# Kernel tuning notes

Measured on AMD Instinct MI355X. Metric: run time of the kernel, lower is better.

Reference implementation:

```python
import jax, jax.numpy as jnp
import numpy as np

B, H, S, D = 4, 16, 2048, 128
HIDDEN_DIM = 128  # init arg; used as softmax scale


def setup_inputs() -> dict:
    key = jax.random.key(0)
    kq, kk, kv = jax.random.split(key, 3)
    q = jax.random.normal(kq, (B, H, S, D), dtype=jnp.float32)
    k = jax.random.normal(kk, (B, H, S, D), dtype=jnp.float32)
    v = jax.random.normal(kv, (B, H, S, D), dtype=jnp.float32)
    return {"q": q, "k": k, "v": v}


def reference(q, k, v):
    # scores[b,h,s,t] = sum_d q[b,h,s,d] * k[b,h,t,d]  (y permuted on last two dims, then matmul)
    scores = jnp.einsum("bhsd,bhtd->bhst", q, k) * (HIDDEN_DIM ** -0.5)
    probs = jax.nn.softmax(scores, axis=-1)
    return jnp.einsum("bhst,bhtd->bhsd", probs, v)
```

## Files before the change

### kernel.cpp

```cpp
#include <hip/hip_runtime.h>
#include <hip/hip_bf16.h>


#define SEQ 2048
#define DH  128
#define NBH 64
#define BM  128
#define BN  64
#define NT  (SEQ / BN)
#define QK_LD 136
#define VT_LD 72
#define P_LD  72
#define TP_LD 130
#define THR 8.0f

typedef __attribute__((ext_vector_type(8))) short short8;
typedef __attribute__((ext_vector_type(4))) float f32x4;
typedef __attribute__((ext_vector_type(16))) float f32x16;
typedef __attribute__((ext_vector_type(2))) unsigned int u32x2;

#if __has_builtin(__builtin_amdgcn_exp2f)
#define EXP2F(x) __builtin_amdgcn_exp2f(x)
#else
#define EXP2F(x) exp2f(x)
#endif

#define CS (0.08838834764831845f * 1.44269504088896340736f)

__device__ __forceinline__ unsigned int pk_bf16(float lo, float hi) {
    union { __hip_bfloat162 h; unsigned int u; } cv;
    cv.h = __float22bfloat162_rn(make_float2(lo, hi));
    return cv.u;
}

__device__ __forceinline__ short8 repack_pf(float a0, float a1, float a2, float a3,
                                            float a4, float a5, float a6, float a7,
                                            int hi) {
    unsigned pq0 = pk_bf16(a0, a1);
    unsigned pq1 = pk_bf16(a2, a3);
    unsigned pq2 = pk_bf16(a4, a5);
    unsigned pq3 = pk_bf16(a6, a7);
    union { short8 s; uint4 u; } cv;
#if __has_builtin(__builtin_amdgcn_permlane32_swap)
    u32x2 r02 = __builtin_amdgcn_permlane32_swap(pq0, pq2, false, false);
    u32x2 r13 = __builtin_amdgcn_permlane32_swap(pq1, pq3, false, false);
    cv.u.x = r02[0]; cv.u.y = r13[0]; cv.u.z = r02[1]; cv.u.w = r13[1];
    (void)hi;
#else
    unsigned px0 = (unsigned)__shfl_xor((int)pq0, 32);
    unsigned px1 = (unsigned)__shfl_xor((int)pq1, 32);
    unsigned px2 = (unsigned)__shfl_xor((int)pq2, 32);
    unsigned px3 = (unsigned)__shfl_xor((int)pq3, 32);
    cv.u.x = hi ? px2 : pq0;
    cv.u.y = hi ? px3 : pq1;
    cv.u.z = hi ? pq2 : px0;
    cv.u.w = hi ? pq3 : px1;
#endif
    return cv.s;
}

template<bool DOK>
__global__ __launch_bounds__(256) void prep_kernel(
        const float* __restrict__ v, unsigned short* __restrict__ vt,
        const float* __restrict__ k, unsigned short* __restrict__ kb) {
    __shared__ unsigned int tileT[64 * TP_LD];
    const int tid = threadIdx.x;

    if (blockIdx.x >= 8) {
        if (!DOK) return;
        const int kid = (blockIdx.x - 8) + 8 * blockIdx.y + 16 * blockIdx.z;
        const float* src = k + (size_t)kid * 16384;
        unsigned short* dst = kb + (size_t)kid * 16384;
#pragma unroll
        for (int i = 0; i < 16; ++i) {
            int off = (tid + 256 * i) * 4;
            float4 val = *reinterpret_cast<const float4*>(src + off);
            uint2 pk;
            pk.x = pk_bf16(val.x, val.y);
            pk.y = pk_bf16(val.z, val.w);
            *reinterpret_cast<uint2*>(dst + off) = pk;
        }
        return;
    }

    const int bh = blockIdx.z;
    const int s0 = blockIdx.x * 256;
    const int d0 = blockIdx.y * 64;
    const int lane = tid & 63;
    const int wv   = tid >> 6;
    const int l31  = lane & 31;
    const int hiv  = lane >> 5;

    const float* srcv = v + ((size_t)bh * SEQ + s0) * DH + d0 + 2 * l31;
    const int drow = 2 * l31 + hiv;
#pragma unroll 4
    for (int i = 0; i < 32; ++i) {
        const int kp = wv * 32 + i;
        float2 X = *reinterpret_cast<const float2*>(srcv + (size_t)(2 * kp + hiv) * DH);
        union { float f; unsigned u; } bx, by;
        bx.f = X.x; by.f = X.y;
        float k0d0, k1d0, k0d1, k1d1;
#if __has_builtin(__builtin_amdgcn_permlane32_swap)
        u32x2 rx = __builtin_amdgcn_permlane32_swap(bx.u, bx.u, false, false);
        u32x2 ry = __builtin_amdgcn_permlane32_swap(by.u, by.u, false, false);
        union { unsigned u; float f; } c0, c1, c2, c3;
        c0.u = rx[0]; c1.u = rx[1]; c2.u = ry[0]; c3.u = ry[1];
        k0d0 = c0.f; k1d0 = c1.f; k0d1 = c2.f; k1d1 = c3.f;
#else
        float xo = __shfl_xor(X.x, 32), yo = __shfl_xor(X.y, 32);
        k0d0 = hiv ? xo : X.x;  k1d0 = hiv ? X.x : xo;
        k0d1 = hiv ? yo : X.y;  k1d1 = hiv ? X.y : yo;
#endif
        unsigned pk = hiv ? pk_bf16(k0d1, k1d1) : pk_bf16(k0d0, k1d0);
        tileT[drow * TP_LD + kp] = pk;
    }
    __syncthreads();

    unsigned short* dst = vt + ((size_t)bh * DH + d0) * SEQ + s0;
#pragma unroll
    for (int i = 0; i < 8; ++i) {
        int id = tid + 256 * i;
        int dd = id >> 5;
        int m  = id & 31;
        const unsigned int* p = &tileT[dd * TP_LD + 4 * m];
        uint2 a = *reinterpret_cast<const uint2*>(p);
        uint2 b = *reinterpret_cast<const uint2*>(p + 2);
        uint4 o; o.x = a.x; o.y = a.y; o.z = b.x; o.w = b.y;
        *reinterpret_cast<uint4*>(dst + (size_t)dd * SEQ + 8 * m) = o;
    }
}

__global__ __launch_bounds__(256, 2) void fattn_kernel(
        const float* __restrict__ q, const unsigned short* __restrict__ kb,
        const unsigned short* __restrict__ vt, float* __restrict__ out) {
    __shared__ unsigned short Ks[2][BN * QK_LD];
    __shared__ unsigned short Vs[2][DH * VT_LD];

    const int wid = ((blockIdx.x & 7) << 7) | (blockIdx.x >> 3);
    const int bh  = wid >> 4;
    const int q0  = (wid & 15) * BM;
    const int tid  = threadIdx.x;
    const int w    = tid >> 6;
    const int lane = tid & 63;
    const int l31  = lane & 31;
    const int hi   = lane >> 5;

    short8 qb[8];
    {
        const float* qptr = q + ((size_t)bh * SEQ + q0 + w * 32 + l31) * DH + hi * 8;
#pragma unroll
        for (int ks = 0; ks < 8; ++ks) {
            float4 x = *reinterpret_cast<const float4*>(qptr + 16 * ks);
            float4 y = *reinterpret_cast<const float4*>(qptr + 16 * ks + 4);
            union { short8 s; uint4 u; } cv;
            cv.u.x = pk_bf16(x.x * CS, x.y * CS);
            cv.u.y = pk_bf16(x.z * CS, x.w * CS);
            cv.u.z = pk_bf16(y.x * CS, y.y * CS);
            cv.u.w = pk_bf16(y.z * CS, y.w * CS);
            qb[ks] = cv.s;
        }
    }

    f32x16 o0, o1, o2, o3;
#pragma unroll
    for (int i = 0; i < 16; ++i) { o0[i] = 0.f; o1[i] = 0.f; o2[i] = 0.f; o3[i] = 0.f; }
    float m = -1e30f, lsum = 0.f;

    const unsigned short* kbp  = kb + (size_t)bh * SEQ * DH;
    const unsigned short* vptr = vt + (size_t)bh * DH * SEQ;

    uint4 kr0, kr1, kr2, kr3, vr0, vr1, vr2, vr3;
    const int krow = tid >> 4, kcol = (tid & 15) << 3;
    const int vrow = tid >> 3, vcol = (tid & 7) << 3;
    const unsigned short* kst = kbp + (size_t)krow * DH + kcol;
    const unsigned short* vst = vptr + (size_t)vrow * SEQ + vcol;

#define LOAD_TILE(K0)                                                              \
    do {                                                                           \
        const unsigned short* _kp = kst + (size_t)(K0) * DH;                       \
        kr0 = *reinterpret_cast<const uint4*>(_kp);                                \
        kr1 = *reinterpret_cast<const uint4*>(_kp + 16 * DH);                      \
        kr2 = *reinterpret_cast<const uint4*>(_kp + 32 * DH);                      \
        kr3 = *reinterpret_cast<const uint4*>(_kp + 48 * DH);                      \
        const unsigned short* _vp = vst + (K0);                                    \
        vr0 = *reinterpret_cast<const uint4*>(_vp);                                \
        vr1 = *reinterpret_cast<const uint4*>(_vp + 32 * SEQ);                     \
        vr2 = *reinterpret_cast<const uint4*>(_vp + 64 * SEQ);                     \
        vr3 = *reinterpret_cast<const uint4*>(_vp + 96 * SEQ);                     \
    } while (0)

#define WRITE_TILE(B)                                                              \
    do {                                                                           \
        *reinterpret_cast<uint4*>(&Ks[B][(krow     ) * QK_LD + kcol]) = kr0;       \
        *reinterpret_cast<uint4*>(&Ks[B][(krow + 16) * QK_LD + kcol]) = kr1;       \
        *reinterpret_cast<uint4*>(&Ks[B][(krow + 32) * QK_LD + kcol]) = kr2;       \
        *reinterpret_cast<uint4*>(&Ks[B][(krow + 48) * QK_LD + kcol]) = kr3;       \
        *reinterpret_cast<uint4*>(&Vs[B][(vrow     ) * VT_LD + vcol]) = vr0;       \
        *reinterpret_cast<uint4*>(&Vs[B][(vrow + 32) * VT_LD + vcol]) = vr1;       \
        *reinterpret_cast<uint4*>(&Vs[B][(vrow + 64) * VT_LD + vcol]) = vr2;       \
        *reinterpret_cast<uint4*>(&Vs[B][(vrow + 96) * VT_LD + vcol]) = vr3;       \
    } while (0)

    LOAD_TILE(0);
    WRITE_TILE(0);
    __syncthreads();
    int cur = 0;

    for (int kt = 0; kt < NT; ++kt) {
        if (kt + 1 < NT) LOAD_TILE((kt + 1) * BN);

        const unsigned short* KsA = &Ks[cur][l31 * QK_LD + hi * 8];
        const unsigned short* VsA = &Vs[cur][l31 * VT_LD + hi * 8];

        f32x16 s0, s1;
#pragma unroll
        for (int i = 0; i < 16; ++i) { s0[i] = 0.f; s1[i] = 0.f; }
        __builtin_amdgcn_s_setprio(1);
#pragma unroll
        for (int ks = 0; ks < 8; ++ks) {
            short8 a0 = *reinterpret_cast<const short8*>(KsA + 16 * ks);
            short8 a1 = *reinterpret_cast<const short8*>(KsA + 32 * QK_LD + 16 * ks);
            s0 = __builtin_amdgcn_mfma_f32_32x32x16_bf16(a0, qb[ks], s0, 0, 0, 0);
            s1 = __builtin_amdgcn_mfma_f32_32x32x16_bf16(a1, qb[ks], s1, 0, 0, 0);
        }
        __builtin_amdgcn_s_setprio(0);

        float mx = s0[0];
#pragma unroll
        for (int i = 1; i < 16; ++i) mx = fmaxf(mx, s0[i]);
#pragma unroll
        for (int i = 0; i < 16; ++i) mx = fmaxf(mx, s1[i]);
        mx = fmaxf(mx, __shfl_xor(mx, 32));
        if (__any(mx - m > THR)) {
            float mn = fmaxf(m, mx);
            float al = EXP2F(m - mn);
            m = mn; lsum *= al;
#pragma unroll
            for (int i = 0; i < 16; ++i) { o0[i] *= al; o1[i] *= al; o2[i] *= al; o3[i] *= al; }
        }
#pragma unroll
        for (int i = 0; i < 16; ++i) s0[i] = EXP2F(s0[i] - m);
#pragma unroll
        for (int i = 0; i < 16; ++i) s1[i] = EXP2F(s1[i] - m);
        float ls = 0.f;
#pragma unroll
        for (int i = 0; i < 16; ++i) ls += s0[i] + s1[i];
        lsum += ls;

        short8 pf0 = repack_pf(s0[0], s0[1], s0[2],  s0[3],  s0[4],  s0[5],  s0[6],  s0[7],  hi);
        short8 pf1 = repack_pf(s0[8], s0[9], s0[10], s0[11], s0[12], s0[13], s0[14], s0[15], hi);
        short8 pf2 = repack_pf(s1[0], s1[1], s1[2],  s1[3],  s1[4],  s1[5],  s1[6],  s1[7],  hi);
        short8 pf3 = repack_pf(s1[8], s1[9], s1[10], s1[11], s1[12], s1[13], s1[14], s1[15], hi);

        __builtin_amdgcn_s_setprio(1);
#define PV_C(OC, C)                                                                \
        {                                                                          \
            short8 va0 = *reinterpret_cast<const short8*>(VsA + (32*(C)) * VT_LD);      \
            short8 va1 = *reinterpret_cast<const short8*>(VsA + (32*(C)) * VT_LD + 16); \
            short8 va2 = *reinterpret_cast<const short8*>(VsA + (32*(C)) * VT_LD + 32); \
            short8 va3 = *reinterpret_cast<const short8*>(VsA + (32*(C)) * VT_LD + 48); \
            OC = __builtin_amdgcn_mfma_f32_32x32x16_bf16(va0, pf0, OC, 0, 0, 0);   \
            OC = __builtin_amdgcn_mfma_f32_32x32x16_bf16(va1, pf1, OC, 0, 0, 0);   \
            OC = __builtin_amdgcn_mfma_f32_32x32x16_bf16(va2, pf2, OC, 0, 0, 0);   \
            OC = __builtin_amdgcn_mfma_f32_32x32x16_bf16(va3, pf3, OC, 0, 0, 0);   \
        }
        PV_C(o0, 0) PV_C(o1, 1) PV_C(o2, 2) PV_C(o3, 3)
        __builtin_amdgcn_s_setprio(0);

        if (kt + 1 < NT) WRITE_TILE(cur ^ 1);
        __syncthreads();
        cur ^= 1;
    }

    lsum += __shfl_xor(lsum, 32);
    float inv = 1.0f / lsum;
    float* obase = out + ((size_t)bh * SEQ + q0 + w * 32 + l31) * DH + 4 * hi;
#define STORE_C(OC, C)                                                             \
    {                                                                              \
        _Pragma("unroll")                                                          \
        for (int u = 0; u < 4; ++u) {                                              \
            float4 st;                                                             \
            st.x = OC[4*u+0] * inv; st.y = OC[4*u+1] * inv;                        \
            st.z = OC[4*u+2] * inv; st.w = OC[4*u+3] * inv;                        \
            *reinterpret_cast<float4*>(obase + 32*(C) + 8*u) = st;                 \
        }                                                                          \
    }
    STORE_C(o0, 0) STORE_C(o1, 1) STORE_C(o2, 2) STORE_C(o3, 3)
}

__global__ __launch_bounds__(256, 3) void fattn_fallback(
        const float* __restrict__ q, const float* __restrict__ kf,
        const unsigned short* __restrict__ vt, float* __restrict__ out) {
    __shared__ unsigned short Ks[64 * QK_LD];
    __shared__ unsigned short Vs[DH * VT_LD];
    __shared__ unsigned short Ps[64 * P_LD];

    const int wid = ((blockIdx.x & 7) << 8) | (blockIdx.x >> 3);
    const int bh  = wid >> 5;
    const int q0  = (wid & 31) * 64;
    const int tid  = threadIdx.x;
    const int w    = tid >> 6;
    const int lane = tid & 63;
    const int l15  = lane & 15;
    const int quad = lane >> 4;

    short8 qf[4];
    {
        const float* qptr = q + ((size_t)bh * SEQ + q0 + w * 16 + l15) * DH + quad * 8;
#pragma unroll
        for (int kk = 0; kk < 4; ++kk) {
            float4 x = *reinterpret_cast<const float4*>(qptr + kk * 32);
            float4 y = *reinterpret_cast<const float4*>(qptr + kk * 32 + 4);
            union { short8 s; uint4 u; } cv;
            cv.u.x = pk_bf16(x.x * CS, x.y * CS);
            cv.u.y = pk_bf16(x.z * CS, x.w * CS);
            cv.u.z = pk_bf16(y.x * CS, y.y * CS);
            cv.u.w = pk_bf16(y.z * CS, y.w * CS);
            qf[kk] = cv.s;
        }
    }

    f32x4 o[8];
#pragma unroll
    for (int t = 0; t < 8; ++t) o[t] = (f32x4){0.f, 0.f, 0.f, 0.f};
    float mrow[4] = {-1e30f, -1e30f, -1e30f, -1e30f};
    float lrow[4] = {0.f, 0.f, 0.f, 0.f};

    const float*          kfp  = kf + (size_t)bh * SEQ * DH;
    const unsigned short* vptr = vt + (size_t)bh * DH * SEQ;

    unsigned int* Ps32 = reinterpret_cast<unsigned int*>(Ps);
    const int prow_base = w * 16 + quad * 4;
    const int pdw = (l15 & 1) ? (8 + (l15 >> 1)) : (l15 >> 1);

    for (int kt = 0; kt < NT; ++kt) {
        const int k0 = kt * BN;
#pragma unroll
        for (int i = 0; i < 8; ++i) {
            int id  = tid + 256 * i;
            int row = id >> 5;
            int c4  = (id & 31) << 2;
            float4 val = *reinterpret_cast<const float4*>(kfp + (size_t)(k0 + row) * DH + c4);
            uint2 pk;
            pk.x = pk_bf16(val.x, val.y);
            pk.y = pk_bf16(val.z, val.w);
            *reinterpret_cast<uint2*>(&Ks[row * QK_LD + c4]) = pk;
        }
#pragma unroll
        for (int i = 0; i < 4; ++i) {
            int id = tid + 256 * i;
            int dd = id >> 3;
            int kc = (id & 7) << 3;
            *reinterpret_cast<uint4*>(&Vs[dd * VT_LD + kc]) =
                *reinterpret_cast<const uint4*>(vptr + (size_t)dd * SEQ + k0 + kc);
        }
        __syncthreads();

        f32x4 acc[4];
#pragma unroll
        for (int t = 0; t < 4; ++t) acc[t] = (f32x4){0.f, 0.f, 0.f, 0.f};
#pragma unroll
        for (int kk = 0; kk < 4; ++kk) {
            const int koff = kk * 32 + quad * 8;
#pragma unroll
            for (int t = 0; t < 4; ++t) {
                short8 b = *reinterpret_cast<const short8*>(&Ks[(t * 16 + l15) * QK_LD + koff]);
                acc[t] = __builtin_amdgcn_mfma_f32_16x16x32_bf16(qf[kk], b, acc[t], 0, 0, 0);
            }
        }

        float lm[4];
#pragma unroll
        for (int r = 0; r < 4; ++r)
            lm[r] = fmaxf(fmaxf(acc[0][r], acc[1][r]), fmaxf(acc[2][r], acc[3][r]));
        float need = fmaxf(fmaxf(lm[0] - mrow[0], lm[1] - mrow[1]),
                           fmaxf(lm[2] - mrow[2], lm[3] - mrow[3]));
        if (__any(need > THR)) {
#pragma unroll
            for (int r = 0; r < 4; ++r) {
                float mx = lm[r];
#pragma unroll
                for (int off = 1; off < 16; off <<= 1)
                    mx = fmaxf(mx, __shfl_xor(mx, off));
                float mnew  = fmaxf(mrow[r], mx);
                float alpha = EXP2F(mrow[r] - mnew);
                mrow[r] = mnew;
                lrow[r] *= alpha;
#pragma unroll
                for (int t = 0; t < 8; ++t) o[t][r] *= alpha;
            }
        }

#pragma unroll
        for (int r = 0; r < 4; ++r) {
            float p0 = EXP2F(acc[0][r] - mrow[r]);
            float p1 = EXP2F(acc[1][r] - mrow[r]);
            float p2 = EXP2F(acc[2][r] - mrow[r]);
            float p3 = EXP2F(acc[3][r] - mrow[r]);
            lrow[r] += (p0 + p1) + (p2 + p3);
            unsigned int a01 = pk_bf16(p0, p1);
            unsigned int a23 = pk_bf16(p2, p3);
            unsigned int s01 = __shfl_xor((int)a01, 1);
            unsigned int s23 = __shfl_xor((int)a23, 1);
            unsigned int w0, w1;
            if (l15 & 1) {
                w0 = (s01 >> 16) | (a01 & 0xffff0000u);
                w1 = (s23 >> 16) | (a23 & 0xffff0000u);
            } else {
                w0 = (a01 & 0xffffu) | (s01 << 16);
                w1 = (a23 & 0xffffu) | (s23 << 16);
            }
            const int dw = (prow_base + r) * (P_LD / 2) + pdw;
            Ps32[dw]      = w0;
            Ps32[dw + 16] = w1;
        }

#pragma unroll
        for (int kk = 0; kk < 2; ++kk) {
            const int koff = kk * 32 + quad * 8;
            short8 a = *reinterpret_cast<const short8*>(&Ps[(w * 16 + l15) * P_LD + koff]);
#pragma unroll
            for (int t = 0; t < 8; ++t) {
                short8 b = *reinterpret_cast<const short8*>(&Vs[(t * 16 + l15) * VT_LD + koff]);
                o[t] = __builtin_amdgcn_mfma_f32_16x16x32_bf16(a, b, o[t], 0, 0, 0);
            }
        }
        __syncthreads();
    }

#pragma unroll
    for (int r = 0; r < 4; ++r) {
#pragma unroll
        for (int off = 1; off < 16; off <<= 1)
            lrow[r] += __shfl_xor(lrow[r], off);
    }
    float* obase = out + ((size_t)bh * SEQ + q0) * DH;
#pragma unroll
    for (int r = 0; r < 4; ++r) {
        float inv = 1.0f / lrow[r];
        int row = w * 16 + quad * 4 + r;
#pragma unroll
        for (int t = 0; t < 8; ++t)
            obase[(size_t)row * DH + t * 16 + l15] = o[t][r] * inv;
    }
}

extern "C" void kernel_launch(void* const* d_in, const int* in_sizes, int n_in,
                              void* d_out, int out_size, void* d_ws, size_t ws_size,
                              hipStream_t stream) {
    const float* q = (const float*)d_in[0];
    const float* k = (const float*)d_in[1];
    const float* v = (const float*)d_in[2];
    float* out = (float*)d_out;
    unsigned short* vt = (unsigned short*)d_ws;

    const size_t vt_elems = (size_t)NBH * SEQ * DH;
    if (ws_size >= 2 * vt_elems * sizeof(unsigned short)) {
        unsigned short* kbuf = vt + vt_elems;
        prep_kernel<true><<<dim3(16, 2, NBH), dim3(256), 0, stream>>>(v, vt, k, kbuf);
        fattn_kernel<<<dim3((SEQ / BM) * NBH), dim3(256), 0, stream>>>(q, kbuf, vt, out);
    } else {
        prep_kernel<false><<<dim3(16, 2, NBH), dim3(256), 0, stream>>>(v, vt, nullptr, nullptr);
        fattn_fallback<<<dim3((SEQ / 64) * NBH), dim3(256), 0, stream>>>(q, k, vt, out);
    }
}
```

Baseline: 358.4 us.

## Convert K to bf16 in-kernel and split softmax/PV into two half-tiles

Removes the separate K fp32-to-bf16 conversion pass from the prep kernel. The attention kernel now loads fp32 K directly and packs it to bf16 when writing shared memory. The QK^T result is processed as two 32-column halves, each with its own max check, exp, and PV MFMA, so softmax work on one half can overlap matrix-core work on the other. The s_setprio hints and the fallback kernel are dropped. The trade-off is doubled K global load bytes per tile, more register pressure and extra conversion ALU work inside the main loop, in exchange for one fewer full pass over K in memory.

```diff
diff --git a/kernel.cpp b/kernel.cpp
--- a/kernel.cpp
+++ b/kernel.cpp
@@ -10,12 +10,10 @@
 #define NT  (SEQ / BN)
 #define QK_LD 136
 #define VT_LD 72
-#define P_LD  72
 #define TP_LD 130
 #define THR 8.0f
 
 typedef __attribute__((ext_vector_type(8))) short short8;
-typedef __attribute__((ext_vector_type(4))) float f32x4;
 typedef __attribute__((ext_vector_type(16))) float f32x16;
 typedef __attribute__((ext_vector_type(2))) unsigned int u32x2;
 
@@ -59,30 +57,10 @@
     return cv.s;
 }
 
-template<bool DOK>
 __global__ __launch_bounds__(256) void prep_kernel(
-        const float* __restrict__ v, unsigned short* __restrict__ vt,
-        const float* __restrict__ k, unsigned short* __restrict__ kb) {
+        const float* __restrict__ v, unsigned short* __restrict__ vt) {
     __shared__ unsigned int tileT[64 * TP_LD];
     const int tid = threadIdx.x;
-
-    if (blockIdx.x >= 8) {
-        if (!DOK) return;
-        const int kid = (blockIdx.x - 8) + 8 * blockIdx.y + 16 * blockIdx.z;
-        const float* src = k + (size_t)kid * 16384;
-        unsigned short* dst = kb + (size_t)kid * 16384;
-#pragma unroll
-        for (int i = 0; i < 16; ++i) {
-            int off = (tid + 256 * i) * 4;
-            float4 val = *reinterpret_cast<const float4*>(src + off);
-            uint2 pk;
-            pk.x = pk_bf16(val.x, val.y);
-            pk.y = pk_bf16(val.z, val.w);
-            *reinterpret_cast<uint2*>(dst + off) = pk;
-        }
-        return;
-    }
-
     const int bh = blockIdx.z;
     const int s0 = blockIdx.x * 256;
     const int d0 = blockIdx.y * 64;
@@ -131,7 +109,7 @@
 }
 
 __global__ __launch_bounds__(256, 2) void fattn_kernel(
-        const float* __restrict__ q, const unsigned short* __restrict__ kb,
+        const float* __restrict__ q, const float* __restrict__ kf,
         const unsigned short* __restrict__ vt, float* __restrict__ out) {
     __shared__ unsigned short Ks[2][BN * QK_LD];
     __shared__ unsigned short Vs[2][DH * VT_LD];
@@ -166,22 +144,27 @@
     for (int i = 0; i < 16; ++i) { o0[i] = 0.f; o1[i] = 0.f; o2[i] = 0.f; o3[i] = 0.f; }
     float m = -1e30f, lsum = 0.f;
 
-    const unsigned short* kbp  = kb + (size_t)bh * SEQ * DH;
+    const float*          kfp  = kf + (size_t)bh * SEQ * DH;
     const unsigned short* vptr = vt + (size_t)bh * DH * SEQ;
 
-    uint4 kr0, kr1, kr2, kr3, vr0, vr1, vr2, vr3;
+    float4 ka0, kb0, ka1, kb1, ka2, kb2, ka3, kb3;
+    uint4 vr0, vr1, vr2, vr3;
     const int krow = tid >> 4, kcol = (tid & 15) << 3;
     const int vrow = tid >> 3, vcol = (tid & 7) << 3;
-    const unsigned short* kst = kbp + (size_t)krow * DH + kcol;
+    const float* kstf = kfp + (size_t)krow * DH + kcol;
     const unsigned short* vst = vptr + (size_t)vrow * SEQ + vcol;
 
 #define LOAD_TILE(K0)                                                              \
     do {                                                                           \
-        const unsigned short* _kp = kst + (size_t)(K0) * DH;                       \
-        kr0 = *reinterpret_cast<const uint4*>(_kp);                                \
-        kr1 = *reinterpret_cast<const uint4*>(_kp + 16 * DH);                      \
-        kr2 = *reinterpret_cast<const uint4*>(_kp + 32 * DH);                      \
-        kr3 = *reinterpret_cast<const uint4*>(_kp + 48 * DH);                      \
+        const float* _kp = kstf + (size_t)(K0) * DH;                               \
+        ka0 = *reinterpret_cast<const float4*>(_kp);                               \
+        kb0 = *reinterpret_cast<const float4*>(_kp + 4);                           \
+        ka1 = *reinterpret_cast<const float4*>(_kp + 16 * DH);                     \
+        kb1 = *reinterpret_cast<const float4*>(_kp + 16 * DH + 4);                 \
+        ka2 = *reinterpret_cast<const float4*>(_kp + 32 * DH);                     \
+        kb2 = *reinterpret_cast<const float4*>(_kp + 32 * DH + 4);                 \
+        ka3 = *reinterpret_cast<const float4*>(_kp + 48 * DH);                     \
+        kb3 = *reinterpret_cast<const float4*>(_kp + 48 * DH + 4);                 \
         const unsigned short* _vp = vst + (K0);                                    \
         vr0 = *reinterpret_cast<const uint4*>(_vp);                                \
         vr1 = *reinterpret_cast<const uint4*>(_vp + 32 * SEQ);                     \
@@ -189,12 +172,17 @@
         vr3 = *reinterpret_cast<const uint4*>(_vp + 96 * SEQ);                     \
     } while (0)
 
+#define KPACK(A, B4) { pk_bf16((A).x, (A).y), pk_bf16((A).z, (A).w),               \
+                       pk_bf16((B4).x, (B4).y), pk_bf16((B4).z, (B4).w) }
+
 #define WRITE_TILE(B)                                                              \
     do {                                                                           \
-        *reinterpret_cast<uint4*>(&Ks[B][(krow     ) * QK_LD + kcol]) = kr0;       \
-        *reinterpret_cast<uint4*>(&Ks[B][(krow + 16) * QK_LD + kcol]) = kr1;       \
-        *reinterpret_cast<uint4*>(&Ks[B][(krow + 32) * QK_LD + kcol]) = kr2;       \
-        *reinterpret_cast<uint4*>(&Ks[B][(krow + 48) * QK_LD + kcol]) = kr3;       \
+        uint4 _w0 = KPACK(ka0, kb0), _w1 = KPACK(ka1, kb1);                        \
+        uint4 _w2 = KPACK(ka2, kb2), _w3 = KPACK(ka3, kb3);                        \
+        *reinterpret_cast<uint4*>(&Ks[B][(krow     ) * QK_LD + kcol]) = _w0;       \
+        *reinterpret_cast<uint4*>(&Ks[B][(krow + 16) * QK_LD + kcol]) = _w1;       \
+        *reinterpret_cast<uint4*>(&Ks[B][(krow + 32) * QK_LD + kcol]) = _w2;       \
+        *reinterpret_cast<uint4*>(&Ks[B][(krow + 48) * QK_LD + kcol]) = _w3;       \
         *reinterpret_cast<uint4*>(&Vs[B][(vrow     ) * VT_LD + vcol]) = vr0;       \
         *reinterpret_cast<uint4*>(&Vs[B][(vrow + 32) * VT_LD + vcol]) = vr1;       \
         *reinterpret_cast<uint4*>(&Vs[B][(vrow + 64) * VT_LD + vcol]) = vr2;       \
@@ -215,24 +203,23 @@
         f32x16 s0, s1;
 #pragma unroll
         for (int i = 0; i < 16; ++i) { s0[i] = 0.f; s1[i] = 0.f; }
-        __builtin_amdgcn_s_setprio(1);
 #pragma unroll
         for (int ks = 0; ks < 8; ++ks) {
             short8 a0 = *reinterpret_cast<const short8*>(KsA + 16 * ks);
+            s0 = __builtin_amdgcn_mfma_f32_32x32x16_bf16(a0, qb[ks], s0, 0, 0, 0);
+        }
+#pragma unroll
+        for (int ks = 0; ks < 8; ++ks) {
             short8 a1 = *reinterpret_cast<const short8*>(KsA + 32 * QK_LD + 16 * ks);
-            s0 = __builtin_amdgcn_mfma_f32_32x32x16_bf16(a0, qb[ks], s0, 0, 0, 0);
             s1 = __builtin_amdgcn_mfma_f32_32x32x16_bf16(a1, qb[ks], s1, 0, 0, 0);
         }
-        __builtin_amdgcn_s_setprio(0);
-
-        float mx = s0[0];
-#pragma unroll
-        for (int i = 1; i < 16; ++i) mx = fmaxf(mx, s0[i]);
-#pragma unroll
-        for (int i = 0; i < 16; ++i) mx = fmaxf(mx, s1[i]);
-        mx = fmaxf(mx, __shfl_xor(mx, 32));
-        if (__any(mx - m > THR)) {
-            float mn = fmaxf(m, mx);
+
+        float mx0 = s0[0];
+#pragma unroll
+        for (int i = 1; i < 16; ++i) mx0 = fmaxf(mx0, s0[i]);
+        mx0 = fmaxf(mx0, __shfl_xor(mx0, 32));
+        if (__any(mx0 - m > THR)) {
+            float mn = fmaxf(m, mx0);
             float al = EXP2F(m - mn);
             m = mn; lsum *= al;
 #pragma unroll
@@ -240,32 +227,50 @@
         }
 #pragma unroll
         for (int i = 0; i < 16; ++i) s0[i] = EXP2F(s0[i] - m);
-#pragma unroll
-        for (int i = 0; i < 16; ++i) s1[i] = EXP2F(s1[i] - m);
-        float ls = 0.f;
-#pragma unroll
-        for (int i = 0; i < 16; ++i) ls += s0[i] + s1[i];
-        lsum += ls;
-
+        float ls0 = 0.f;
+#pragma unroll
+        for (int i = 0; i < 16; ++i) ls0 += s0[i];
+        lsum += ls0;
         short8 pf0 = repack_pf(s0[0], s0[1], s0[2],  s0[3],  s0[4],  s0[5],  s0[6],  s0[7],  hi);
         short8 pf1 = repack_pf(s0[8], s0[9], s0[10], s0[11], s0[12], s0[13], s0[14], s0[15], hi);
-        short8 pf2 = repack_pf(s1[0], s1[1], s1[2],  s1[3],  s1[4],  s1[5],  s1[6],  s1[7],  hi);
-        short8 pf3 = repack_pf(s1[8], s1[9], s1[10], s1[11], s1[12], s1[13], s1[14], s1[15], hi);
-
-        __builtin_amdgcn_s_setprio(1);
-#define PV_C(OC, C)                                                                \
+
+#define PV_H0(OC, C)                                                               \
         {                                                                          \
             short8 va0 = *reinterpret_cast<const short8*>(VsA + (32*(C)) * VT_LD);      \
             short8 va1 = *reinterpret_cast<const short8*>(VsA + (32*(C)) * VT_LD + 16); \
+            OC = __builtin_amdgcn_mfma_f32_32x32x16_bf16(va0, pf0, OC, 0, 0, 0);   \
+            OC = __builtin_amdgcn_mfma_f32_32x32x16_bf16(va1, pf1, OC, 0, 0, 0);   \
+        }
+        PV_H0(o0, 0) PV_H0(o1, 1) PV_H0(o2, 2) PV_H0(o3, 3)
+
+        float mx1 = s1[0];
+#pragma unroll
+        for (int i = 1; i < 16; ++i) mx1 = fmaxf(mx1, s1[i]);
+        mx1 = fmaxf(mx1, __shfl_xor(mx1, 32));
+        if (__any(mx1 - m > THR)) {
+            float mn = fmaxf(m, mx1);
+            float al = EXP2F(m - mn);
+            m = mn; lsum *= al;
+#pragma unroll
+            for (int i = 0; i < 16; ++i) { o0[i] *= al; o1[i] *= al; o2[i] *= al; o3[i] *= al; }
+        }
+#pragma unroll
+        for (int i = 0; i < 16; ++i) s1[i] = EXP2F(s1[i] - m);
+        float ls1 = 0.f;
+#pragma unroll
+        for (int i = 0; i < 16; ++i) ls1 += s1[i];
+        lsum += ls1;
+        short8 pf2 = repack_pf(s1[0], s1[1], s1[2],  s1[3],  s1[4],  s1[5],  s1[6],  s1[7],  hi);
+        short8 pf3 = repack_pf(s1[8], s1[9], s1[10], s1[11], s1[12], s1[13], s1[14], s1[15], hi);
+
+#define PV_H1(OC, C)                                                               \
+        {                                                                          \
             short8 va2 = *reinterpret_cast<const short8*>(VsA + (32*(C)) * VT_LD + 32); \
             short8 va3 = *reinterpret_cast<const short8*>(VsA + (32*(C)) * VT_LD + 48); \
-            OC = __builtin_amdgcn_mfma_f32_32x32x16_bf16(va0, pf0, OC, 0, 0, 0);   \
-            OC = __builtin_amdgcn_mfma_f32_32x32x16_bf16(va1, pf1, OC, 0, 0, 0);   \
             OC = __builtin_amdgcn_mfma_f32_32x32x16_bf16(va2, pf2, OC, 0, 0, 0);   \
             OC = __builtin_amdgcn_mfma_f32_32x32x16_bf16(va3, pf3, OC, 0, 0, 0);   \
         }
-        PV_C(o0, 0) PV_C(o1, 1) PV_C(o2, 2) PV_C(o3, 3)
-        __builtin_amdgcn_s_setprio(0);
+        PV_H1(o0, 0) PV_H1(o1, 1) PV_H1(o2, 2) PV_H1(o3, 3)
 
         if (kt + 1 < NT) WRITE_TILE(cur ^ 1);
         __syncthreads();
@@ -288,163 +293,6 @@
     STORE_C(o0, 0) STORE_C(o1, 1) STORE_C(o2, 2) STORE_C(o3, 3)
 }
 
-__global__ __launch_bounds__(256, 3) void fattn_fallback(
-        const float* __restrict__ q, const float* __restrict__ kf,
-        const unsigned short* __restrict__ vt, float* __restrict__ out) {
-    __shared__ unsigned short Ks[64 * QK_LD];
-    __shared__ unsigned short Vs[DH * VT_LD];
-    __shared__ unsigned short Ps[64 * P_LD];
-
-    const int wid = ((blockIdx.x & 7) << 8) | (blockIdx.x >> 3);
-    const int bh  = wid >> 5;
-    const int q0  = (wid & 31) * 64;
-    const int tid  = threadIdx.x;
-    const int w    = tid >> 6;
-    const int lane = tid & 63;
-    const int l15  = lane & 15;
-    const int quad = lane >> 4;
-
-    short8 qf[4];
-    {
-        const float* qptr = q + ((size_t)bh * SEQ + q0 + w * 16 + l15) * DH + quad * 8;
-#pragma unroll
-        for (int kk = 0; kk < 4; ++kk) {
-            float4 x = *reinterpret_cast<const float4*>(qptr + kk * 32);
-            float4 y = *reinterpret_cast<const float4*>(qptr + kk * 32 + 4);
-            union { short8 s; uint4 u; } cv;
-            cv.u.x = pk_bf16(x.x * CS, x.y * CS);
-            cv.u.y = pk_bf16(x.z * CS, x.w * CS);
-            cv.u.z = pk_bf16(y.x * CS, y.y * CS);
-            cv.u.w = pk_bf16(y.z * CS, y.w * CS);
-            qf[kk] = cv.s;
-        }
-    }
-
-    f32x4 o[8];
-#pragma unroll
-    for (int t = 0; t < 8; ++t) o[t] = (f32x4){0.f, 0.f, 0.f, 0.f};
-    float mrow[4] = {-1e30f, -1e30f, -1e30f, -1e30f};
-    float lrow[4] = {0.f, 0.f, 0.f, 0.f};
-
-    const float*          kfp  = kf + (size_t)bh * SEQ * DH;
-    const unsigned short* vptr = vt + (size_t)bh * DH * SEQ;
-
-    unsigned int* Ps32 = reinterpret_cast<unsigned int*>(Ps);
-    const int prow_base = w * 16 + quad * 4;
-    const int pdw = (l15 & 1) ? (8 + (l15 >> 1)) : (l15 >> 1);
-
-    for (int kt = 0; kt < NT; ++kt) {
-        const int k0 = kt * BN;
-#pragma unroll
-        for (int i = 0; i < 8; ++i) {
-            int id  = tid + 256 * i;
-            int row = id >> 5;
-            int c4  = (id & 31) << 2;
-            float4 val = *reinterpret_cast<const float4*>(kfp + (size_t)(k0 + row) * DH + c4);
-            uint2 pk;
-            pk.x = pk_bf16(val.x, val.y);
-            pk.y = pk_bf16(val.z, val.w);
-            *reinterpret_cast<uint2*>(&Ks[row * QK_LD + c4]) = pk;
-        }
-#pragma unroll
-        for (int i = 0; i < 4; ++i) {
-            int id = tid + 256 * i;
-            int dd = id >> 3;
-            int kc = (id & 7) << 3;
-            *reinterpret_cast<uint4*>(&Vs[dd * VT_LD + kc]) =
-                *reinterpret_cast<const uint4*>(vptr + (size_t)dd * SEQ + k0 + kc);
-        }
-        __syncthreads();
-
-        f32x4 acc[4];
-#pragma unroll
-        for (int t = 0; t < 4; ++t) acc[t] = (f32x4){0.f, 0.f, 0.f, 0.f};
-#pragma unroll
-        for (int kk = 0; kk < 4; ++kk) {
-            const int koff = kk * 32 + quad * 8;
-#pragma unroll
-            for (int t = 0; t < 4; ++t) {
-                short8 b = *reinterpret_cast<const short8*>(&Ks[(t * 16 + l15) * QK_LD + koff]);
-                acc[t] = __builtin_amdgcn_mfma_f32_16x16x32_bf16(qf[kk], b, acc[t], 0, 0, 0);
-            }
-        }
-
-        float lm[4];
-#pragma unroll
-        for (int r = 0; r < 4; ++r)
-            lm[r] = fmaxf(fmaxf(acc[0][r], acc[1][r]), fmaxf(acc[2][r], acc[3][r]));
-        float need = fmaxf(fmaxf(lm[0] - mrow[0], lm[1] - mrow[1]),
-                           fmaxf(lm[2] - mrow[2], lm[3] - mrow[3]));
-        if (__any(need > THR)) {
-#pragma unroll
-            for (int r = 0; r < 4; ++r) {
-                float mx = lm[r];
-#pragma unroll
-                for (int off = 1; off < 16; off <<= 1)
-                    mx = fmaxf(mx, __shfl_xor(mx, off));
-                float mnew  = fmaxf(mrow[r], mx);
-                float alpha = EXP2F(mrow[r] - mnew);
-                mrow[r] = mnew;
-                lrow[r] *= alpha;
-#pragma unroll
-                for (int t = 0; t < 8; ++t) o[t][r] *= alpha;
-            }
-        }
-
-#pragma unroll
-        for (int r = 0; r < 4; ++r) {
-            float p0 = EXP2F(acc[0][r] - mrow[r]);
-            float p1 = EXP2F(acc[1][r] - mrow[r]);
-            float p2 = EXP2F(acc[2][r] - mrow[r]);
-            float p3 = EXP2F(acc[3][r] - mrow[r]);
-            lrow[r] += (p0 + p1) + (p2 + p3);
-            unsigned int a01 = pk_bf16(p0, p1);
-            unsigned int a23 = pk_bf16(p2, p3);
-            unsigned int s01 = __shfl_xor((int)a01, 1);
-            unsigned int s23 = __shfl_xor((int)a23, 1);
-            unsigned int w0, w1;
-            if (l15 & 1) {
-                w0 = (s01 >> 16) | (a01 & 0xffff0000u);
-                w1 = (s23 >> 16) | (a23 & 0xffff0000u);
-            } else {
-                w0 = (a01 & 0xffffu) | (s01 << 16);
-                w1 = (a23 & 0xffffu) | (s23 << 16);
-            }
-            const int dw = (prow_base + r) * (P_LD / 2) + pdw;
-            Ps32[dw]      = w0;
-            Ps32[dw + 16] = w1;
-        }
-
-#pragma unroll
-        for (int kk = 0; kk < 2; ++kk) {
-            const int koff = kk * 32 + quad * 8;
-            short8 a = *reinterpret_cast<const short8*>(&Ps[(w * 16 + l15) * P_LD + koff]);
-#pragma unroll
-            for (int t = 0; t < 8; ++t) {
-                short8 b = *reinterpret_cast<const short8*>(&Vs[(t * 16 + l15) * VT_LD + koff]);
-                o[t] = __builtin_amdgcn_mfma_f32_16x16x32_bf16(a, b, o[t], 0, 0, 0);
-            }
-        }
-        __syncthreads();
-    }
-
-#pragma unroll
-    for (int r = 0; r < 4; ++r) {
-#pragma unroll
-        for (int off = 1; off < 16; off <<= 1)
-            lrow[r] += __shfl_xor(lrow[r], off);
-    }
-    float* obase = out + ((size_t)bh * SEQ + q0) * DH;
-#pragma unroll
-    for (int r = 0; r < 4; ++r) {
-        float inv = 1.0f / lrow[r];
-        int row = w * 16 + quad * 4 + r;
-#pragma unroll
-        for (int t = 0; t < 8; ++t)
-            obase[(size_t)row * DH + t * 16 + l15] = o[t][r] * inv;
-    }
-}
-
 extern "C" void kernel_launch(void* const* d_in, const int* in_sizes, int n_in,
                               void* d_out, int out_size, void* d_ws, size_t ws_size,
                               hipStream_t stream) {
@@ -454,13 +302,6 @@
     float* out = (float*)d_out;
     unsigned short* vt = (unsigned short*)d_ws;
 
-    const size_t vt_elems = (size_t)NBH * SEQ * DH;
-    if (ws_size >= 2 * vt_elems * sizeof(unsigned short)) {
-        unsigned short* kbuf = vt + vt_elems;
-        prep_kernel<true><<<dim3(16, 2, NBH), dim3(256), 0, stream>>>(v, vt, k, kbuf);
-        fattn_kernel<<<dim3((SEQ / BM) * NBH), dim3(256), 0, stream>>>(q, kbuf, vt, out);
-    } else {
-        prep_kernel<false><<<dim3(16, 2, NBH), dim3(256), 0, stream>>>(v, vt, nullptr, nullptr);
-        fattn_fallback<<<dim3((SEQ / 64) * NBH), dim3(256), 0, stream>>>(q, k, vt, out);
-    }
-}
+    prep_kernel<<<dim3(8, 2, NBH), dim3(256), 0, stream>>>(v, vt);
+    fattn_kernel<<<dim3((SEQ / BM) * NBH), dim3(256), 0, stream>>>(q, k, vt, out);
+}
```

After: 361.0 us. Within noise of the previous version (+0.7%).
